# Performance work log

Measured on AMD Instinct MI355X. Metric: run time of the kernel, lower is better.

## Reference

```python
import jax, jax.numpy as jnp
import numpy as np

B, D, VOCAB = 8192, 256, 1000000


def setup_inputs() -> dict:
    key = jax.random.key(0)
    k1, k2, k3, k4 = jax.random.split(key, 4)
    input_emb = jax.random.normal(k1, (B, D), dtype=jnp.float32)
    target_emb = jax.random.normal(k2, (B, D), dtype=jnp.float32)
    target_ids = jax.random.randint(k3, (B, 1), 0, VOCAB, dtype=jnp.int64)
    # sampling probabilities must lie strictly in (0,1)
    q_probas = jax.random.uniform(k4, (B,), dtype=jnp.float32) * 0.98 + 0.01
    return {"input_emb": input_emb, "target_emb": target_emb,
            "target_ids": target_ids, "q_probas": q_probas}


def reference(input_emb, target_emb, target_ids, q_probas):
    # sim: [B, B] in-batch similarity
    sim = input_emb @ target_emb.T
    n = q_probas.shape[0]
    # miss[i, j] = True where target j is a valid negative for row i
    miss = target_ids != target_ids.T                      # [B, B] bool
    n_miss = jnp.sum(miss, axis=1, keepdims=True).astype(sim.dtype)  # [B, 1]
    pos_sim = jnp.diagonal(sim)                            # [B]
    # logQ correction: log(n_miss * q_j / (1 - q_i)), broadcast to [B, B]
    correction = jnp.log(n_miss * q_probas[None, :] / (1.0 - q_probas[:, None]))
    mask = miss & (~jnp.eye(n, dtype=bool))                # exclude diagonal
    neg_exp = jnp.where(mask, jnp.exp(sim - correction), 0.0)  # [B, B]
    pos_exp = jnp.exp(pos_sim)
    batch_loss = jnp.mean(-pos_sim + jnp.log(pos_exp + jnp.sum(neg_exp, axis=1)))
    return batch_loss
```

## Files before the change

### kernel.cpp

```cpp
#include <hip/hip_runtime.h>
#include <hip/hip_bf16.h>
#include <stdint.h>

#define MB 8192
#define KD 256
#define BM 128
#define BN 64
#define NSPLIT 8
#define SLAB (MB / NSPLIT)
#define NCHUNK (SLAB / BN)
#define VOCAB 1000000
#define COFF 104.0f
#define LOG2E 1.44269504088896340736f

typedef __attribute__((ext_vector_type(8))) short bf16x8;
typedef __attribute__((ext_vector_type(4))) float f32x4;

__device__ __forceinline__ unsigned short f2bf(float x) {
  union { float f; uint32_t u; } v; v.f = x;
  uint32_t r = v.u + 0x7fffu + ((v.u >> 16) & 1u);
  return (unsigned short)(r >> 16);
}

__device__ __forceinline__ float fast_exp2(float x) {
#if __has_builtin(__builtin_amdgcn_exp2f)
  return __builtin_amdgcn_exp2f(x);
#else
  return exp2f(x);
#endif
}

#define GLOAD_LDS16(g, l)                                                      \
  __builtin_amdgcn_global_load_lds(                                            \
      (const __attribute__((address_space(1))) void*)(g),                      \
      (__attribute__((address_space(3))) void*)(l), 16, 0, 0)

__global__ __launch_bounds__(256) void convertpos_kernel(
    const float* __restrict__ A, const float* __restrict__ B,
    unsigned short* __restrict__ Abf, unsigned short* __restrict__ Bbf,
    float* __restrict__ pos, int* __restrict__ hist) {
  int t = blockIdx.x * 256 + threadIdx.x;
  const float4 a = ((const float4*)A)[t];
  const float4 b = ((const float4*)B)[t];
  ushort4 oa, ob;
  oa.x = f2bf(a.x); oa.y = f2bf(a.y); oa.z = f2bf(a.z); oa.w = f2bf(a.w);
  ob.x = f2bf(b.x); ob.y = f2bf(b.y); ob.z = f2bf(b.z); ob.w = f2bf(b.w);
  ((ushort4*)Abf)[t] = oa;
  ((ushort4*)Bbf)[t] = ob;
  float d = a.x * b.x + a.y * b.y + a.z * b.z + a.w * b.w;
  #pragma unroll
  for (int off = 32; off; off >>= 1) d += __shfl_down(d, off, 64);
  if ((threadIdx.x & 63) == 0) pos[t >> 6] = d;
  ((uint2*)hist)[t] = make_uint2(0u, 0u);
}

__global__ __launch_bounds__(256) void histb2_kernel(
    const int* __restrict__ ids, const float* __restrict__ q,
    int* __restrict__ hist, float* __restrict__ b2,
    float* __restrict__ ps, float* __restrict__ out) {
  int i = blockIdx.x * 256 + threadIdx.x;
  atomicAdd(&hist[ids[i]], 1);
  b2[i] = -(log2f(q[i]) + COFF * LOG2E);
  ps[i] = 0.0f;
  if (i == 0) out[0] = 0.0f;
}

__global__ __launch_bounds__(256, 2) void fused_kernel(
    const unsigned short* __restrict__ Abf,
    const unsigned short* __restrict__ Bbf,
    const int* __restrict__ ids,
    const float* __restrict__ b2,
    float* __restrict__ ps) {
  const int slab = blockIdx.y;
  const int tid = threadIdx.x;
  const int wave = tid >> 6;
  const int lane = tid & 63;
  const int quad = lane >> 4;
  const int lpos = lane & 15;
  const int rowbase = blockIdx.x * BM + wave * 32;
  const int colbase = slab * SLAB;

  __shared__ unsigned short Bs[2][2048 * 8];

  bf16x8 afrag[2][8];
  #pragma unroll
  for (int rt = 0; rt < 2; ++rt)
    #pragma unroll
    for (int kb = 0; kb < 8; ++kb)
      afrag[rt][kb] = *(const bf16x8*)(Abf + (rowbase + rt * 16 + lpos) * KD + kb * 32 + quad * 8);

  const unsigned short* gsrc[8];
  int ldso[8];
  #pragma unroll
  for (int s8 = 0; s8 < 8; ++s8) {
    int c = tid + s8 * 256;
    int lp = c & 15, qd = (c >> 4) & 3, kb = (c >> 6) & 7, ct = c >> 9;
    gsrc[s8] = Bbf + (colbase + ct * 16 + lp) * KD + kb * 32 + qd * 8;
    ldso[s8] = c * 8;
  }

  int idr[2][4];
  float srun[2][4];
  #pragma unroll
  for (int rt = 0; rt < 2; ++rt)
    #pragma unroll
    for (int r = 0; r < 4; ++r) {
      idr[rt][r] = ids[rowbase + rt * 16 + quad * 4 + r];
      srun[rt][r] = 0.0f;
    }

  int idv[2][4];
  float bv[2][4];
  #pragma unroll
  for (int ct = 0; ct < 4; ++ct) {
    idv[0][ct] = ids[colbase + ct * 16 + lpos];
    bv[0][ct]  = b2 [colbase + ct * 16 + lpos];
  }
  #pragma unroll
  for (int s8 = 0; s8 < 8; ++s8)
    GLOAD_LDS16(gsrc[s8], &Bs[0][0] + ldso[s8]);
  __syncthreads();

#define FUSED_BODY(T, CUR)                                                     \
  {                                                                            \
    const int nxt = (T) + 1;                                                   \
    if (nxt < NCHUNK) {                                                        \
      _Pragma("unroll")                                                        \
      for (int ct = 0; ct < 4; ++ct) {                                         \
        idv[(CUR) ^ 1][ct] = ids[colbase + nxt * BN + ct * 16 + lpos];         \
        bv[(CUR) ^ 1][ct]  = b2 [colbase + nxt * BN + ct * 16 + lpos];         \
      }                                                                        \
      _Pragma("unroll")                                                        \
      for (int s8 = 0; s8 < 8; ++s8)                                           \
        GLOAD_LDS16(gsrc[s8] + nxt * (BN * KD), &Bs[(CUR) ^ 1][0] + ldso[s8]); \
    }                                                                          \
    _Pragma("unroll")                                                          \
    for (int ct = 0; ct < 4; ++ct) {                                           \
      const unsigned short* bp = &Bs[CUR][0] + (ct * 512 + quad * 16 + lpos) * 8; \
      bf16x8 bfrag[8];                                                         \
      _Pragma("unroll")                                                        \
      for (int kb = 0; kb < 8; ++kb)                                           \
        bfrag[kb] = *(const bf16x8*)(bp + kb * 512);                           \
      const int idj = idv[CUR][ct];                                            \
      const float bj = bv[CUR][ct];                                            \
      _Pragma("unroll")                                                        \
      for (int rt = 0; rt < 2; ++rt) {                                         \
        f32x4 acc = {0.0f, 0.0f, 0.0f, 0.0f};                                  \
        _Pragma("unroll")                                                      \
        for (int kb = 0; kb < 8; ++kb)                                         \
          acc = __builtin_amdgcn_mfma_f32_16x16x32_bf16(afrag[rt][kb], bfrag[kb], acc, 0, 0, 0); \
        _Pragma("unroll")                                                      \
        for (int r = 0; r < 4; ++r) {                                          \
          const float e = fast_exp2(__builtin_fmaf(acc[r], LOG2E, bj));        \
          srun[rt][r] += (idj != idr[rt][r]) ? e : 0.0f;                       \
        }                                                                      \
      }                                                                        \
    }                                                                          \
    __syncthreads();                                                           \
  }

  for (int t2 = 0; t2 < NCHUNK; t2 += 2) {
    FUSED_BODY(t2, 0)
    FUSED_BODY(t2 + 1, 1)
  }
#undef FUSED_BODY

  #pragma unroll
  for (int rt = 0; rt < 2; ++rt)
    #pragma unroll
    for (int r = 0; r < 4; ++r) {
      float v = srun[rt][r];
      #pragma unroll
      for (int off = 1; off < 16; off <<= 1) v += __shfl_xor(v, off, 64);
      if (lpos == 0)
        atomicAdd(&ps[rowbase + rt * 16 + quad * 4 + r], v);
    }
}

__global__ __launch_bounds__(256) void finalize_kernel(
    const float* __restrict__ ps, const float* __restrict__ pos,
    const float* __restrict__ q, const int* __restrict__ ids,
    const int* __restrict__ hist, float* __restrict__ out) {
  int i = blockIdx.x * 256 + threadIdx.x;
  const float s = ps[i];
  const float nm = (float)(MB - hist[ids[i]]);
  const float z = logf(s) + COFF + logf(1.0f - q[i]) - logf(nm);
  const float p = pos[i];
  const float hi = fmaxf(p, z), lo = fminf(p, z);
  float loss = -p + hi + log1pf(__expf(lo - hi));

  #pragma unroll
  for (int off = 32; off; off >>= 1) loss += __shfl_down(loss, off, 64);
  __shared__ float red[4];
  if ((threadIdx.x & 63) == 0) red[threadIdx.x >> 6] = loss;
  __syncthreads();
  if (threadIdx.x == 0) {
    float t = red[0] + red[1] + red[2] + red[3];
    atomicAdd(out, t * (1.0f / (float)MB));
  }
}

extern "C" void kernel_launch(void* const* d_in, const int* in_sizes, int n_in,
                              void* d_out, int out_size, void* d_ws, size_t ws_size,
                              hipStream_t stream) {
  (void)in_sizes; (void)n_in; (void)out_size; (void)ws_size;
  const float* input_emb  = (const float*)d_in[0];
  const float* target_emb = (const float*)d_in[1];
  const int*   target_ids = (const int*)d_in[2];
  const float* q_probas   = (const float*)d_in[3];
  float* out = (float*)d_out;

  char* ws = (char*)d_ws;
  unsigned short* Abf = (unsigned short*)(ws);
  unsigned short* Bbf = (unsigned short*)(ws + (4u << 20));
  int*   hist = (int*)  (ws + (8u << 20));
  float* b2   = (float*)(ws + (12u << 20));
  float* pos  = (float*)(ws + (12u << 20) + 32768);
  float* ps   = (float*)(ws + (12u << 20) + 65536);

  convertpos_kernel<<<2048, 256, 0, stream>>>(input_emb, target_emb, Abf, Bbf, pos, hist);
  histb2_kernel<<<32, 256, 0, stream>>>(target_ids, q_probas, hist, b2, ps, out);
  fused_kernel<<<dim3(MB / BM, NSPLIT), 256, 0, stream>>>(Abf, Bbf, target_ids, b2, ps);
  finalize_kernel<<<32, 256, 0, stream>>>(ps, pos, q_probas, target_ids, hist, out);
}
```

Measured before the change: 119.5 us.

## Count duplicate ids inside fused GEMM loop and drop histogram kernel

Replaces the 4MB vocabulary histogram (zeroed in the convert kernel and filled by a separate atomic kernel) with a per-row count of matching ids, accumulated inside the fused similarity/exp loop and reduced with atomics alongside the row sums. The b2/ps/out initialization moves into the prep kernel, so the pipeline goes from four launches to three and no longer writes 4MB of zeros. In exchange the hot loop does an extra compare-and-add per element and a second shuffle reduction plus atomic per row at the end.

New measurement: 119.8 us. No clear change (+0.3%).

```diff
diff --git a/kernel.cpp b/kernel.cpp
--- a/kernel.cpp
+++ b/kernel.cpp
@@ -9,7 +9,6 @@
 #define NSPLIT 8
 #define SLAB (MB / NSPLIT)
 #define NCHUNK (SLAB / BN)
-#define VOCAB 1000000
 #define COFF 104.0f
 #define LOG2E 1.44269504088896340736f
 
@@ -35,10 +34,13 @@
       (const __attribute__((address_space(1))) void*)(g),                      \
       (__attribute__((address_space(3))) void*)(l), 16, 0, 0)
 
-__global__ __launch_bounds__(256) void convertpos_kernel(
+__global__ __launch_bounds__(256) void prep_kernel(
     const float* __restrict__ A, const float* __restrict__ B,
+    const float* __restrict__ q,
     unsigned short* __restrict__ Abf, unsigned short* __restrict__ Bbf,
-    float* __restrict__ pos, int* __restrict__ hist) {
+    float* __restrict__ pos, float* __restrict__ b2,
+    float* __restrict__ ps, float* __restrict__ cnt,
+    float* __restrict__ out) {
   int t = blockIdx.x * 256 + threadIdx.x;
   const float4 a = ((const float4*)A)[t];
   const float4 b = ((const float4*)B)[t];
@@ -51,18 +53,12 @@
   #pragma unroll
   for (int off = 32; off; off >>= 1) d += __shfl_down(d, off, 64);
   if ((threadIdx.x & 63) == 0) pos[t >> 6] = d;
-  ((uint2*)hist)[t] = make_uint2(0u, 0u);
-}
-
-__global__ __launch_bounds__(256) void histb2_kernel(
-    const int* __restrict__ ids, const float* __restrict__ q,
-    int* __restrict__ hist, float* __restrict__ b2,
-    float* __restrict__ ps, float* __restrict__ out) {
-  int i = blockIdx.x * 256 + threadIdx.x;
-  atomicAdd(&hist[ids[i]], 1);
-  b2[i] = -(log2f(q[i]) + COFF * LOG2E);
-  ps[i] = 0.0f;
-  if (i == 0) out[0] = 0.0f;
+  if (t < MB) {
+    b2[t] = -(log2f(q[t]) + COFF * LOG2E);
+    ps[t] = 0.0f;
+    cnt[t] = 0.0f;
+    if (t == 0) out[0] = 0.0f;
+  }
 }
 
 __global__ __launch_bounds__(256, 2) void fused_kernel(
@@ -70,7 +66,7 @@
     const unsigned short* __restrict__ Bbf,
     const int* __restrict__ ids,
     const float* __restrict__ b2,
-    float* __restrict__ ps) {
+    float* __restrict__ ps, float* __restrict__ cnt) {
   const int slab = blockIdx.y;
   const int tid = threadIdx.x;
   const int wave = tid >> 6;
@@ -101,12 +97,14 @@
 
   int idr[2][4];
   float srun[2][4];
+  float crun[2][4];
   #pragma unroll
   for (int rt = 0; rt < 2; ++rt)
     #pragma unroll
     for (int r = 0; r < 4; ++r) {
       idr[rt][r] = ids[rowbase + rt * 16 + quad * 4 + r];
       srun[rt][r] = 0.0f;
+      crun[rt][r] = 0.0f;
     }
 
   int idv[2][4];
@@ -151,8 +149,10 @@
           acc = __builtin_amdgcn_mfma_f32_16x16x32_bf16(afrag[rt][kb], bfrag[kb], acc, 0, 0, 0); \
         _Pragma("unroll")                                                      \
         for (int r = 0; r < 4; ++r) {                                          \
+          const bool eq = (idj == idr[rt][r]);                                 \
           const float e = fast_exp2(__builtin_fmaf(acc[r], LOG2E, bj));        \
-          srun[rt][r] += (idj != idr[rt][r]) ? e : 0.0f;                       \
+          srun[rt][r] += eq ? 0.0f : e;                                        \
+          crun[rt][r] += eq ? 1.0f : 0.0f;                                     \
         }                                                                      \
       }                                                                        \
     }                                                                          \
@@ -170,20 +170,26 @@
     #pragma unroll
     for (int r = 0; r < 4; ++r) {
       float v = srun[rt][r];
+      float c = crun[rt][r];
       #pragma unroll
-      for (int off = 1; off < 16; off <<= 1) v += __shfl_xor(v, off, 64);
-      if (lpos == 0)
+      for (int off = 1; off < 16; off <<= 1) {
+        v += __shfl_xor(v, off, 64);
+        c += __shfl_xor(c, off, 64);
+      }
+      if (lpos == 0) {
         atomicAdd(&ps[rowbase + rt * 16 + quad * 4 + r], v);
+        atomicAdd(&cnt[rowbase + rt * 16 + quad * 4 + r], c);
+      }
     }
 }
 
 __global__ __launch_bounds__(256) void finalize_kernel(
     const float* __restrict__ ps, const float* __restrict__ pos,
-    const float* __restrict__ q, const int* __restrict__ ids,
-    const int* __restrict__ hist, float* __restrict__ out) {
+    const float* __restrict__ q, const float* __restrict__ cnt,
+    float* __restrict__ out) {
   int i = blockIdx.x * 256 + threadIdx.x;
   const float s = ps[i];
-  const float nm = (float)(MB - hist[ids[i]]);
+  const float nm = (float)MB - cnt[i];
   const float z = logf(s) + COFF + logf(1.0f - q[i]) - logf(nm);
   const float p = pos[i];
   const float hi = fmaxf(p, z), lo = fminf(p, z);
@@ -213,13 +219,14 @@
   char* ws = (char*)d_ws;
   unsigned short* Abf = (unsigned short*)(ws);
   unsigned short* Bbf = (unsigned short*)(ws + (4u << 20));
-  int*   hist = (int*)  (ws + (8u << 20));
-  float* b2   = (float*)(ws + (12u << 20));
-  float* pos  = (float*)(ws + (12u << 20) + 32768);
-  float* ps   = (float*)(ws + (12u << 20) + 65536);
-
-  convertpos_kernel<<<2048, 256, 0, stream>>>(input_emb, target_emb, Abf, Bbf, pos, hist);
-  histb2_kernel<<<32, 256, 0, stream>>>(target_ids, q_probas, hist, b2, ps, out);
-  fused_kernel<<<dim3(MB / BM, NSPLIT), 256, 0, stream>>>(Abf, Bbf, target_ids, b2, ps);
-  finalize_kernel<<<32, 256, 0, stream>>>(ps, pos, q_probas, target_ids, hist, out);
-}
+  float* b2   = (float*)(ws + (8u << 20));
+  float* pos  = (float*)(ws + (8u << 20) + 32768);
+  float* ps   = (float*)(ws + (8u << 20) + 65536);
+  float* cnt  = (float*)(ws + (8u << 20) + 98304);
+
+  prep_kernel<<<2048, 256, 0, stream>>>(input_emb, target_emb, q_probas,
+                                        Abf, Bbf, pos, b2, ps, cnt, out);
+  fused_kernel<<<dim3(MB / BM, NSPLIT), 256, 0, stream>>>(Abf, Bbf, target_ids,
+                                                          b2, ps, cnt);
+  finalize_kernel<<<32, 256, 0, stream>>>(ps, pos, q_probas, cnt, out);
+}
```
